# Kernel tuning notes

Measured on AMD Instinct MI355X. Metric: run time of the kernel, lower is better.

The kernel has to match this reference:

```python
import jax, jax.numpy as jnp
import numpy as np

D_MODEL = 1024
HEADS = 16
D_K = D_MODEL // HEADS
D_FF = 4096
EPS = 1e-5


def _layernorm(x, gamma, beta):
    mu = jnp.mean(x, axis=-1, keepdims=True)
    var = jnp.var(x, axis=-1, keepdims=True)
    return (x - mu) * jax.lax.rsqrt(var + EPS) * gamma + beta


def setup_inputs() -> dict:
    key = jax.random.key(0)
    ks = jax.random.split(key, 8)
    s = 0.02
    return {
        "x": jax.random.normal(ks[0], (4, 2048, D_MODEL), dtype=jnp.float32),
        "wq": jax.random.normal(ks[1], (D_MODEL, D_MODEL), dtype=jnp.float32) * s,
        "wk": jax.random.normal(ks[2], (D_MODEL, D_MODEL), dtype=jnp.float32) * s,
        "wv": jax.random.normal(ks[3], (D_MODEL, D_MODEL), dtype=jnp.float32) * s,
        "wo": jax.random.normal(ks[4], (D_MODEL, D_MODEL), dtype=jnp.float32) * s,
        "w1": jax.random.normal(ks[5], (D_MODEL, D_FF), dtype=jnp.float32) * s,
        "b1": jnp.zeros((D_FF,), dtype=jnp.float32),
        "w2": jax.random.normal(ks[6], (D_FF, D_MODEL), dtype=jnp.float32) * s,
        "b2": jnp.zeros((D_MODEL,), dtype=jnp.float32),
        "g1": jnp.ones((D_MODEL,), dtype=jnp.float32),
        "be1": jnp.zeros((D_MODEL,), dtype=jnp.float32),
        "g2": jnp.ones((D_MODEL,), dtype=jnp.float32),
        "be2": jnp.zeros((D_MODEL,), dtype=jnp.float32),
    }


def reference(x, wq, wk, wv, wo, w1, b1, w2, b2, g1, be1, g2, be2):
    B, S, D = x.shape
    # --- multi-head self-attention (dropout = identity at eval) ---
    q = (x @ wq).reshape(B, S, HEADS, D_K).transpose(0, 2, 1, 3)  # [B,H,S,dk]
    k = (x @ wk).reshape(B, S, HEADS, D_K).transpose(0, 2, 1, 3)
    v = (x @ wv).reshape(B, S, HEADS, D_K).transpose(0, 2, 1, 3)
    scores = jnp.einsum("bhqd,bhkd->bhqk", q, k) / jnp.sqrt(jnp.float32(D_K))
    attn = jax.nn.softmax(scores, axis=-1)
    ctx = jnp.einsum("bhqk,bhkd->bhqd", attn, v)
    ctx = ctx.transpose(0, 2, 1, 3).reshape(B, S, D)
    attn_out = ctx @ wo
    # --- add & norm 1 ---
    h = _layernorm(x + attn_out, g1, be1)
    # --- FFN ---
    ffn = jax.nn.relu(h @ w1 + b1) @ w2 + b2
    # --- add & norm 2 ---
    return _layernorm(h + ffn, g2, be2)
```

## Files before the change

kernel.cpp:

```cpp
#include <hip/hip_runtime.h>
#include <hip/hip_bf16.h>


typedef float  floatx2  __attribute__((ext_vector_type(2)));
typedef float  floatx4  __attribute__((ext_vector_type(4)));
typedef float  floatx16 __attribute__((ext_vector_type(16)));
typedef short  shortx8  __attribute__((ext_vector_type(8)));
typedef short  shortx4  __attribute__((ext_vector_type(4)));
typedef int    intx4    __attribute__((ext_vector_type(4)));
typedef unsigned uintx2 __attribute__((ext_vector_type(2)));

__device__ __forceinline__ short f2bs(float f) {
    union { float f; unsigned u; } a; a.f = f;
    unsigned r = a.u + 0x7fffu + ((a.u >> 16) & 1u);
    return (short)(r >> 16);
}

__device__ __forceinline__ float fexp2(float x) {
#if __has_builtin(__builtin_amdgcn_exp2f)
    return __builtin_amdgcn_exp2f(x);
#else
    return __expf(0.6931471805599453f * x);
#endif
}

__device__ __forceinline__ void lane32swap(unsigned& a, unsigned& b) {
#if __has_builtin(__builtin_amdgcn_permlane32_swap)
    uintx2 r = __builtin_amdgcn_permlane32_swap(a, b, false, false);
    a = r[0]; b = r[1];
#else
    int hl = (threadIdx.x & 63) >> 5;
    unsigned ta = (unsigned)__shfl_xor((int)a, 32);
    unsigned tb = (unsigned)__shfl_xor((int)b, 32);
    unsigned na = hl ? tb : a;
    unsigned nb = hl ? b : ta;
    a = na; b = nb;
#endif
}

__device__ __forceinline__ void gload16(const short* g, short* l) {
    __builtin_amdgcn_global_load_lds(
        (const __attribute__((address_space(1))) void*)g,
        (__attribute__((address_space(3))) void*)l,
        16, 0, 0);
}

#define WAITV(n) asm volatile("s_waitcnt vmcnt(" #n ")" ::: "memory")
#define FENCE    asm volatile("" ::: "memory")

__device__ __forceinline__ void trans_tile(const float* __restrict__ in,
                                           short* __restrict__ out,
                                           int N, int K, int k0, int n0,
                                           short (*t)[68]) {
    const int tid = threadIdx.x;
    const int r = tid >> 4, c4 = (tid & 15) * 4;
#pragma unroll
    for (int i = 0; i < 4; ++i) {
        int k = r + i * 16;
        floatx4 v = *(const floatx4*)(in + (size_t)(k0 + k) * N + n0 + c4);
        shortx4 s;
#pragma unroll
        for (int j = 0; j < 4; ++j) s[j] = f2bs(v[j]);
        *(shortx4*)(&t[k][c4]) = s;
    }
    __syncthreads();
#pragma unroll
    for (int i = 0; i < 4; ++i) {
        int n = r + i * 16;
        shortx4 s;
#pragma unroll
        for (int j = 0; j < 4; ++j) s[j] = t[c4 + j][n];
        *(shortx4*)(out + (size_t)(n0 + n) * K + k0 + c4) = s;
    }
}

__global__ __launch_bounds__(256) void prep_kernel(
    const float* __restrict__ wq, const float* __restrict__ wk,
    const float* __restrict__ wv, const float* __restrict__ wo,
    const float* __restrict__ w1, const float* __restrict__ w2,
    const float* __restrict__ x,
    short* wqt, short* wkt, short* wvt, short* wot,
    short* w1t, short* w2t, short* xb)
{
    __shared__ __align__(16) short t[64][68];
    const int bid = blockIdx.x;
    if (bid < 1024) {
        const int widx = bid >> 8, local = bid & 255;
        const float* in = widx == 0 ? wq : widx == 1 ? wk : widx == 2 ? wv : wo;
        short* out = widx == 0 ? wqt : widx == 1 ? wkt : widx == 2 ? wvt : wot;
        trans_tile(in, out, 1024, 1024, (local & 15) * 64, (local >> 4) * 64, t);
    } else if (bid < 2048) {
        const int local = bid - 1024;
        trans_tile(w1, w1t, 4096, 1024, (local & 15) * 64, (local >> 4) * 64, t);
    } else if (bid < 3072) {
        const int local = bid - 2048;
        trans_tile(w2, w2t, 1024, 4096, (local & 63) * 64, (local >> 6) * 64, t);
    } else {
        const int local = bid - 3072;
#pragma unroll
        for (int j = 0; j < 4; ++j) {
            int i = local * 1024 + j * 256 + threadIdx.x;
            floatx4 v = *(const floatx4*)(x + (size_t)i * 4);
            shortx4 o;
            o[0] = f2bs(v[0]); o[1] = f2bs(v[1]); o[2] = f2bs(v[2]); o[3] = f2bs(v[3]);
            *(shortx4*)(xb + (size_t)i * 4) = o;
        }
    }
}

template<int EPI>
__global__ __launch_bounds__(256) void gemm_bt(
    const short* __restrict__ A, const short* __restrict__ Bt, int K, int N,
    short* __restrict__ outb, float* __restrict__ outf,
    const float* __restrict__ bias, const float* __restrict__ resf)
{
    __shared__ __align__(16) short As[2 * 128 * 32];
    __shared__ __align__(16) short Bs[2 * 128 * 32];
    const int tid = threadIdx.x;
    const int bx = blockIdx.x, by = blockIdx.y;
    const int w = tid >> 6, lane = tid & 63, quad = lane >> 4, l16 = lane & 15;
    const int wm = (w >> 1) * 64, wn = (w & 1) * 64;
    const int lr = lane >> 2, lc = (lane & 3) * 8;
    const short* aSrc = A + (size_t)(by * 128 + w * 32 + lr) * K + lc;
    const short* bSrc = Bt + (size_t)(bx * 128 + w * 32 + lr) * K + lc;
    const size_t k16 = (size_t)16 * K;
    const int wb = w * 32 * 32;

    floatx4 acc[4][4] = {};

    gload16(aSrc, As + wb);
    gload16(aSrc + k16, As + wb + 512);
    gload16(bSrc, Bs + wb);
    gload16(bSrc + k16, Bs + wb + 512);

    int cur = 0;
    for (int k0 = 0; k0 < K; k0 += 32) {
        __syncthreads();
        const int kn = k0 + 32;
        if (kn < K) {
            const int nb = (cur ^ 1) * 4096;
            gload16(aSrc + kn, As + nb + wb);
            gload16(aSrc + k16 + kn, As + nb + wb + 512);
            gload16(bSrc + kn, Bs + nb + wb);
            gload16(bSrc + k16 + kn, Bs + nb + wb + 512);
        }
        const short* Ab = As + cur * 4096;
        const short* Bb = Bs + cur * 4096;
        shortx8 af[4], bf[4];
#pragma unroll
        for (int mt = 0; mt < 4; ++mt)
            af[mt] = *(const shortx8*)(Ab + (wm + mt * 16 + l16) * 32 + quad * 8);
#pragma unroll
        for (int nt = 0; nt < 4; ++nt)
            bf[nt] = *(const shortx8*)(Bb + (wn + nt * 16 + l16) * 32 + quad * 8);
#pragma unroll
        for (int mt = 0; mt < 4; ++mt)
#pragma unroll
            for (int nt = 0; nt < 4; ++nt)
                acc[mt][nt] = __builtin_amdgcn_mfma_f32_16x16x32_bf16(af[mt], bf[nt], acc[mt][nt], 0, 0, 0);
        cur ^= 1;
    }

#pragma unroll
    for (int mt = 0; mt < 4; ++mt) {
#pragma unroll
        for (int nt = 0; nt < 4; ++nt) {
            const int grow0 = by * 128 + wm + mt * 16 + quad * 4;
            const int gcol = bx * 128 + wn + nt * 16 + l16;
#pragma unroll
            for (int r = 0; r < 4; ++r) {
                int grow = grow0 + r;
                float v = acc[mt][nt][r];
                if constexpr (EPI == 1) {
                    v += bias[gcol];
                    v = fmaxf(v, 0.f);
                    outb[(size_t)grow * N + gcol] = f2bs(v);
                } else if constexpr (EPI == 2) {
                    outf[(size_t)grow * N + gcol] = v + resf[(size_t)grow * N + gcol];
                } else if constexpr (EPI == 3) {
                    outf[(size_t)grow * N + gcol] = v + bias[gcol] + resf[(size_t)grow * N + gcol];
                }
            }
        }
    }
}

template<int EPI>
__global__ __launch_bounds__(512, 2) void gemm256(
    const short* __restrict__ A, const short* __restrict__ Bt, const int K, const int N,
    short* __restrict__ outb, float* __restrict__ outf,
    const float* __restrict__ bias, const float* __restrict__ resf)
{
    __shared__ __align__(16) short Ls[65536];
    const int tid = threadIdx.x;
    const int w = tid >> 6, lane = tid & 63;
    const int quad = lane >> 4, l16 = lane & 15;
    const int wm = w >> 2, wn = w & 3;
    const int bx = blockIdx.x, by = blockIdx.y;

    const int srow = w * 16 + (lane >> 3);
    const int uc0 = ((lane & 7) ^ ((lane >> 4) & 7)) * 8;
    const int uc1 = ((lane & 7) ^ (((lane >> 4) + 4) & 7)) * 8;
    const short* aS0 = A  + (size_t)(by * 256 + srow) * K + uc0;
    const short* aS1 = A  + (size_t)(by * 256 + srow + 8) * K + uc1;
    const short* bS0 = Bt + (size_t)(bx * 256 + srow) * K + uc0;
    const short* bS1 = Bt + (size_t)(bx * 256 + srow + 8) * K + uc1;
    const size_t hK = (size_t)128 * K;
    const int wsl = w * 1024;

    const int rswz = (l16 >> 1) & 7;
    const int ru0 = (quad ^ rswz) * 8;
    const int ru1 = ((4 + quad) ^ rswz) * 8;
    const int aRd = (wm * 64 + l16) * 64;
    const int bRd = (wn * 32 + l16) * 64;

    floatx4 acc[8][4] = {};
    shortx8 af[4][2], blo[2][2], bhi[2][2];

#define S_A0(buf, kc) { short* p = Ls + (buf) * 32768 + wsl;         gload16(aS0 + (kc), p);      gload16(aS1 + (kc), p + 512);      FENCE; }
#define S_A1(buf, kc) { short* p = Ls + (buf) * 32768 + 8192 + wsl;  gload16(aS0 + hK + (kc), p); gload16(aS1 + hK + (kc), p + 512); FENCE; }
#define S_B0(buf, kc) { short* p = Ls + (buf) * 32768 + 16384 + wsl; gload16(bS0 + (kc), p);      gload16(bS1 + (kc), p + 512);      FENCE; }
#define S_B1(buf, kc) { short* p = Ls + (buf) * 32768 + 24576 + wsl; gload16(bS0 + hK + (kc), p); gload16(bS1 + hK + (kc), p + 512); FENCE; }
#define MF(a, b, c) c = __builtin_amdgcn_mfma_f32_16x16x32_bf16(a, b, c, 0, 0, 0)

    S_A0(0, 0) S_B0(0, 0) S_B1(0, 0) S_A1(0, 0)

    const int NT = K >> 6;
    for (int t = 0; t < NT - 1; ++t) {
        const int rb = t & 1, wbuf = rb ^ 1, kc = (t + 1) * 64;
        const short* Ab = Ls + rb * 32768;
        const short* Bb = Ab + 16384;
        WAITV(4); __builtin_amdgcn_s_barrier(); FENCE;
#pragma unroll
        for (int mf = 0; mf < 4; ++mf) {
            af[mf][0] = *(const shortx8*)(Ab + aRd + mf * 1024 + ru0);
            af[mf][1] = *(const shortx8*)(Ab + aRd + mf * 1024 + ru1);
        }
#pragma unroll
        for (int nf = 0; nf < 2; ++nf) {
            blo[nf][0] = *(const shortx8*)(Bb + bRd + nf * 1024 + ru0);
            blo[nf][1] = *(const shortx8*)(Bb + bRd + nf * 1024 + ru1);
        }
        S_A0(wbuf, kc)
        __builtin_amdgcn_s_setprio(1);
#pragma unroll
        for (int mf = 0; mf < 4; ++mf)
#pragma unroll
            for (int nf = 0; nf < 2; ++nf) {
                MF(af[mf][0], blo[nf][0], acc[mf][nf]);
                MF(af[mf][1], blo[nf][1], acc[mf][nf]);
            }
        __builtin_amdgcn_s_setprio(0);
        WAITV(4); __builtin_amdgcn_s_barrier(); FENCE;
#pragma unroll
        for (int nf = 0; nf < 2; ++nf) {
            bhi[nf][0] = *(const shortx8*)(Bb + bRd + 8192 + nf * 1024 + ru0);
            bhi[nf][1] = *(const shortx8*)(Bb + bRd + 8192 + nf * 1024 + ru1);
        }
        S_B0(wbuf, kc)
        __builtin_amdgcn_s_setprio(1);
#pragma unroll
        for (int mf = 0; mf < 4; ++mf)
#pragma unroll
            for (int nf = 0; nf < 2; ++nf) {
                MF(af[mf][0], bhi[nf][0], acc[mf][2 + nf]);
                MF(af[mf][1], bhi[nf][1], acc[mf][2 + nf]);
            }
        __builtin_amdgcn_s_setprio(0);
        WAITV(4); __builtin_amdgcn_s_barrier(); FENCE;
#pragma unroll
        for (int mf = 0; mf < 4; ++mf) {
            af[mf][0] = *(const shortx8*)(Ab + aRd + 8192 + mf * 1024 + ru0);
            af[mf][1] = *(const shortx8*)(Ab + aRd + 8192 + mf * 1024 + ru1);
        }
        S_B1(wbuf, kc)
        __builtin_amdgcn_s_setprio(1);
#pragma unroll
        for (int mf = 0; mf < 4; ++mf)
#pragma unroll
            for (int nf = 0; nf < 2; ++nf) {
                MF(af[mf][0], blo[nf][0], acc[4 + mf][nf]);
                MF(af[mf][1], blo[nf][1], acc[4 + mf][nf]);
            }
        __builtin_amdgcn_s_setprio(0);
        S_A1(wbuf, kc)
        __builtin_amdgcn_s_setprio(1);
#pragma unroll
        for (int mf = 0; mf < 4; ++mf)
#pragma unroll
            for (int nf = 0; nf < 2; ++nf) {
                MF(af[mf][0], bhi[nf][0], acc[4 + mf][2 + nf]);
                MF(af[mf][1], bhi[nf][1], acc[4 + mf][2 + nf]);
            }
        __builtin_amdgcn_s_setprio(0);
    }
    {
        const int rb = (NT - 1) & 1;
        const short* Ab = Ls + rb * 32768;
        const short* Bb = Ab + 16384;
        WAITV(4); __builtin_amdgcn_s_barrier(); FENCE;
#pragma unroll
        for (int mf = 0; mf < 4; ++mf) {
            af[mf][0] = *(const shortx8*)(Ab + aRd + mf * 1024 + ru0);
            af[mf][1] = *(const shortx8*)(Ab + aRd + mf * 1024 + ru1);
        }
#pragma unroll
        for (int nf = 0; nf < 2; ++nf) {
            blo[nf][0] = *(const shortx8*)(Bb + bRd + nf * 1024 + ru0);
            blo[nf][1] = *(const shortx8*)(Bb + bRd + nf * 1024 + ru1);
        }
        __builtin_amdgcn_s_setprio(1);
#pragma unroll
        for (int mf = 0; mf < 4; ++mf)
#pragma unroll
            for (int nf = 0; nf < 2; ++nf) {
                MF(af[mf][0], blo[nf][0], acc[mf][nf]);
                MF(af[mf][1], blo[nf][1], acc[mf][nf]);
            }
        __builtin_amdgcn_s_setprio(0);
        WAITV(2); __builtin_amdgcn_s_barrier(); FENCE;
#pragma unroll
        for (int nf = 0; nf < 2; ++nf) {
            bhi[nf][0] = *(const shortx8*)(Bb + bRd + 8192 + nf * 1024 + ru0);
            bhi[nf][1] = *(const shortx8*)(Bb + bRd + 8192 + nf * 1024 + ru1);
        }
        __builtin_amdgcn_s_setprio(1);
#pragma unroll
        for (int mf = 0; mf < 4; ++mf)
#pragma unroll
            for (int nf = 0; nf < 2; ++nf) {
                MF(af[mf][0], bhi[nf][0], acc[mf][2 + nf]);
                MF(af[mf][1], bhi[nf][1], acc[mf][2 + nf]);
            }
        __builtin_amdgcn_s_setprio(0);
        WAITV(0); __builtin_amdgcn_s_barrier(); FENCE;
#pragma unroll
        for (int mf = 0; mf < 4; ++mf) {
            af[mf][0] = *(const shortx8*)(Ab + aRd + 8192 + mf * 1024 + ru0);
            af[mf][1] = *(const shortx8*)(Ab + aRd + 8192 + mf * 1024 + ru1);
        }
        __builtin_amdgcn_s_setprio(1);
#pragma unroll
        for (int mf = 0; mf < 4; ++mf)
#pragma unroll
            for (int nf = 0; nf < 2; ++nf) {
                MF(af[mf][0], blo[nf][0], acc[4 + mf][nf]);
                MF(af[mf][1], blo[nf][1], acc[4 + mf][nf]);
                MF(af[mf][0], bhi[nf][0], acc[4 + mf][2 + nf]);
                MF(af[mf][1], bhi[nf][1], acc[4 + mf][2 + nf]);
            }
        __builtin_amdgcn_s_setprio(0);
    }

#pragma unroll
    for (int mf = 0; mf < 8; ++mf) {
        const int grow0 = by * 256 + (mf >> 2) * 128 + wm * 64 + (mf & 3) * 16 + quad * 4;
#pragma unroll
        for (int nf = 0; nf < 4; ++nf) {
            const int gcol = bx * 256 + (nf >> 1) * 128 + wn * 32 + (nf & 1) * 16 + l16;
            const floatx4 a = acc[mf][nf];
            if constexpr (EPI == 5) {
                const int slice = gcol >> 10, c = gcol & 1023;
                const int hh = c >> 6, d = c & 63;
                const int b = grow0 >> 11, s0 = grow0 & 2047;
                if (slice == 2) {
                    short* vt = outb + ((size_t)16 << 20);
                    shortx4 pkv;
#pragma unroll
                    for (int r = 0; r < 4; ++r) pkv[r] = f2bs(a[r]);
                    *(shortx4*)(vt + ((size_t)((b * 16 + hh) * 64 + d)) * 2048 + s0) = pkv;
                } else {
                    short* dst = slice ? (outb + ((size_t)8 << 20)) : outb;
                    float sc = slice ? 1.f : 0.125f * 1.4426950408889634f;
#pragma unroll
                    for (int r = 0; r < 4; ++r)
                        dst[(((size_t)(b * 16 + hh)) * 2048 + (s0 + r)) * 64 + d] =
                            f2bs(a[r] * sc);
                }
            } else if constexpr (EPI == 1) {
                const float bv = bias[gcol];
#pragma unroll
                for (int r = 0; r < 4; ++r) {
                    float v = fmaxf(a[r] + bv, 0.f);
                    outb[(size_t)(grow0 + r) * N + gcol] = f2bs(v);
                }
            } else if constexpr (EPI == 3) {
                const float bv = bias[gcol];
#pragma unroll
                for (int r = 0; r < 4; ++r)
                    outf[(size_t)(grow0 + r) * N + gcol] =
                        a[r] + bv + resf[(size_t)(grow0 + r) * N + gcol];
            }
        }
    }
#undef S_A0
#undef S_A1
#undef S_B0
#undef S_B1
#undef MF
}

__global__ __launch_bounds__(256) void ln_kernel(
    const float* __restrict__ in, float* __restrict__ outf, short* __restrict__ outb,
    const float* __restrict__ g, const float* __restrict__ be, int writeB)
{
    __shared__ float red[8];
    const int row = blockIdx.x, tid = threadIdx.x;
    const float* p = in + (size_t)row * 1024;
    floatx4 v = *(const floatx4*)(p + tid * 4);
    float s = v[0] + v[1] + v[2] + v[3];
    float q = v[0] * v[0] + v[1] * v[1] + v[2] * v[2] + v[3] * v[3];
#pragma unroll
    for (int off = 32; off; off >>= 1) {
        s += __shfl_xor(s, off);
        q += __shfl_xor(q, off);
    }
    int w = tid >> 6, lane = tid & 63;
    if (lane == 0) { red[w] = s; red[4 + w] = q; }
    __syncthreads();
    s = red[0] + red[1] + red[2] + red[3];
    q = red[4] + red[5] + red[6] + red[7];
    float mean = s * (1.f / 1024.f);
    float var = q * (1.f / 1024.f) - mean * mean;
    float rs = rsqrtf(var + 1e-5f);
    floatx4 gv = *(const floatx4*)(g + tid * 4);
    floatx4 bv = *(const floatx4*)(be + tid * 4);
    floatx4 o4;
#pragma unroll
    for (int i = 0; i < 4; ++i) o4[i] = (v[i] - mean) * rs * gv[i] + bv[i];
    *(floatx4*)(outf + (size_t)row * 1024 + tid * 4) = o4;
    if (writeB) {
        shortx4 ob;
#pragma unroll
        for (int i = 0; i < 4; ++i) ob[i] = f2bs(o4[i]);
        *(shortx4*)(outb + (size_t)row * 1024 + tid * 4) = ob;
    }
}

__global__ __launch_bounds__(256) void attn_kernel(
    const short* __restrict__ Q, const short* __restrict__ K,
    const short* __restrict__ Vt, short* __restrict__ ctx)
{
    __shared__ __align__(16) short Ks[128 * 72];
    __shared__ __align__(16) short Vs[64 * 136];
    const int tid = threadIdx.x;
    const int q0 = blockIdx.x * 128, bh = blockIdx.y;
    const int w = tid >> 6, lane = tid & 63, l31 = lane & 31, hl = lane >> 5;
    const size_t sb = (size_t)bh * 2048 * 64;

    shortx8 qf[4];
#pragma unroll
    for (int ks = 0; ks < 4; ++ks)
        qf[ks] = *(const shortx8*)(Q + sb + (size_t)(q0 + w * 32 + l31) * 64 + ks * 16 + hl * 8);

    const int krow = tid >> 3, kcol = (tid & 7) * 8;
    const int vrow = tid >> 4, vcol = (tid & 15) * 8;

    floatx16 o[2] = {};
    floatx2 rs2 = {0.f, 0.f};

    intx4 kv[4], vv[4];
#pragma unroll
    for (int i = 0; i < 4; ++i) {
        kv[i] = *(const intx4*)(K + sb + (size_t)(i * 32 + krow) * 64 + kcol);
        vv[i] = *(const intx4*)(Vt + sb + (size_t)(i * 16 + vrow) * 2048 + vcol);
    }

    for (int kt = 0; kt < 16; ++kt) {
        __syncthreads();
#pragma unroll
        for (int i = 0; i < 4; ++i) {
            *(intx4*)(Ks + (i * 32 + krow) * 72 + kcol) = kv[i];
            *(intx4*)(Vs + (i * 16 + vrow) * 136 + vcol) = vv[i];
        }
        __syncthreads();
        if (kt < 15) {
            const int kv0 = (kt + 1) * 128;
#pragma unroll
            for (int i = 0; i < 4; ++i) {
                kv[i] = *(const intx4*)(K + sb + (size_t)(kv0 + i * 32 + krow) * 64 + kcol);
                vv[i] = *(const intx4*)(Vt + sb + (size_t)(i * 16 + vrow) * 2048 + kv0 + vcol);
            }
        }

#pragma unroll
        for (int mt = 0; mt < 4; ++mt) {
            floatx16 s = {};
#pragma unroll
            for (int ks = 0; ks < 4; ++ks) {
                shortx8 ak = *(const shortx8*)(Ks + (mt * 32 + l31) * 72 + ks * 16 + hl * 8);
                s = __builtin_amdgcn_mfma_f32_32x32x16_bf16(ak, qf[ks], s, 0, 0, 0);
            }
            floatx2 ps2[8];
#pragma unroll
            for (int i = 0; i < 8; ++i) {
                ps2[i][0] = fexp2(s[2 * i]);
                ps2[i][1] = fexp2(s[2 * i + 1]);
                rs2 += ps2[i];
            }
            unsigned pk[8];
#pragma unroll
            for (int i = 0; i < 8; ++i) {
                union { __hip_bfloat162 h; unsigned u; } cv;
                cv.h = __float22bfloat162_rn(make_float2(ps2[i][0], ps2[i][1]));
                pk[i] = cv.u;
            }
            lane32swap(pk[0], pk[2]);
            lane32swap(pk[1], pk[3]);
            lane32swap(pk[4], pk[6]);
            lane32swap(pk[5], pk[7]);
#pragma unroll
            for (int ksl = 0; ksl < 2; ++ksl) {
                union { unsigned i[4]; shortx8 s8; } fr;
                fr.i[0] = pk[4 * ksl];     fr.i[1] = pk[4 * ksl + 1];
                fr.i[2] = pk[4 * ksl + 2]; fr.i[3] = pk[4 * ksl + 3];
#pragma unroll
                for (int mtd = 0; mtd < 2; ++mtd) {
                    shortx8 av = *(const shortx8*)(Vs + (mtd * 32 + l31) * 136 + mt * 32 + ksl * 16 + hl * 8);
                    o[mtd] = __builtin_amdgcn_mfma_f32_32x32x16_bf16(av, fr.s8, o[mtd], 0, 0, 0);
                }
            }
        }
    }

    float rsum = rs2[0] + rs2[1];
    float tot = rsum + __shfl_xor(rsum, 32);
    float inv = 1.f / tot;

    __syncthreads();
    short* O_lds = Ks;
#pragma unroll
    for (int mtd = 0; mtd < 2; ++mtd)
#pragma unroll
        for (int g = 0; g < 4; ++g) {
            shortx4 p4;
#pragma unroll
            for (int r = 0; r < 4; ++r) p4[r] = f2bs(o[mtd][4 * g + r] * inv);
            *(shortx4*)(O_lds + (w * 32 + l31) * 72 + mtd * 32 + g * 8 + hl * 4) = p4;
        }
    __syncthreads();
    const int b = bh >> 4, head = bh & 15;
#pragma unroll
    for (int it = 0; it < 4; ++it) {
        int idx = it * 256 + tid;
        int q = idx >> 3, ch = idx & 7;
        shortx8 v = *(const shortx8*)(O_lds + q * 72 + ch * 8);
        *(shortx8*)(ctx + ((size_t)(b * 2048 + q0 + q)) * 1024 + head * 64 + ch * 8) = v;
    }
}

extern "C" void kernel_launch(void* const* d_in, const int* in_sizes, int n_in,
                              void* d_out, int out_size, void* d_ws, size_t ws_size,
                              hipStream_t stream) {
    const float* x   = (const float*)d_in[0];
    const float* wq  = (const float*)d_in[1];
    const float* wk  = (const float*)d_in[2];
    const float* wv  = (const float*)d_in[3];
    const float* wo  = (const float*)d_in[4];
    const float* w1  = (const float*)d_in[5];
    const float* b1  = (const float*)d_in[6];
    const float* w2  = (const float*)d_in[7];
    const float* b2  = (const float*)d_in[8];
    const float* g1p = (const float*)d_in[9];
    const float* be1 = (const float*)d_in[10];
    const float* g2p = (const float*)d_in[11];
    const float* be2 = (const float*)d_in[12];
    float* out = (float*)d_out;

    char* ws = (char*)d_ws;
    const size_t MB = 1ull << 20;
    short* wqt  = (short*)(ws + 0 * MB);
    short* wkt  = (short*)(ws + 2 * MB);
    short* wvt  = (short*)(ws + 4 * MB);
    short* wot  = (short*)(ws + 6 * MB);
    short* w1t  = (short*)(ws + 8 * MB);
    short* w2t  = (short*)(ws + 16 * MB);
    short* xb   = (short*)(ws + 24 * MB);
    short* Qb   = (short*)(ws + 40 * MB);
    short* Kb   = (short*)(ws + 56 * MB);
    short* Vtg  = (short*)(ws + 72 * MB);
    short* ctxb = (short*)(ws + 88 * MB);
    float* tf   = (float*)(ws + 104 * MB);
    short* hb   = (short*)(ws + 136 * MB);
    short* f1b  = (short*)(ws + 40 * MB);

    prep_kernel<<<5120, 256, 0, stream>>>(wq, wk, wv, wo, w1, w2, x,
                                          wqt, wkt, wvt, wot, w1t, w2t, xb);

    gemm256<5><<<dim3(12, 32), 512, 0, stream>>>(xb, wqt, 1024, 3072, Qb, nullptr, nullptr, nullptr);
    attn_kernel<<<dim3(16, 64), 256, 0, stream>>>(Qb, Kb, Vtg, ctxb);
    gemm_bt<2><<<dim3(8, 64), 256, 0, stream>>>(ctxb, wot, 1024, 1024, nullptr, tf, nullptr, x);
    ln_kernel<<<8192, 256, 0, stream>>>(tf, tf, hb, g1p, be1, 1);
    gemm256<1><<<dim3(16, 32), 512, 0, stream>>>(hb, w1t, 1024, 4096, f1b, nullptr, b1, nullptr);
    gemm256<3><<<dim3(4, 32), 512, 0, stream>>>(f1b, w2t, 4096, 1024, nullptr, out, b2, tf);
    ln_kernel<<<8192, 256, 0, stream>>>(out, out, nullptr, g2p, be2, 0);
}
```

Baseline: 413.7 us.

## Add 256x128 GEMM tile variant, drop gemm_bt, software-pipeline attention QK MFMAs

Templates the 256-wide GEMM on tile width N and adds a 256x128 variant with its own load schedule. The QKV, output-projection and FFN2 GEMMs switch to it so the grid has more blocks across the CUs, and the output projection moves off the older 128x128 kernel. Separately, the attention kernel computes the next QK score tile while the softmax and PV MFMAs of the current tile run, with setprio hints and split row-sum accumulators. This adds overlap and occupancy but raises register pressure and lowers per-block reuse of A tiles.

```diff
diff --git a/kernel.cpp b/kernel.cpp
--- a/kernel.cpp
+++ b/kernel.cpp
@@ -108,90 +108,15 @@
     }
 }
 
-template<int EPI>
-__global__ __launch_bounds__(256) void gemm_bt(
-    const short* __restrict__ A, const short* __restrict__ Bt, int K, int N,
-    short* __restrict__ outb, float* __restrict__ outf,
-    const float* __restrict__ bias, const float* __restrict__ resf)
-{
-    __shared__ __align__(16) short As[2 * 128 * 32];
-    __shared__ __align__(16) short Bs[2 * 128 * 32];
-    const int tid = threadIdx.x;
-    const int bx = blockIdx.x, by = blockIdx.y;
-    const int w = tid >> 6, lane = tid & 63, quad = lane >> 4, l16 = lane & 15;
-    const int wm = (w >> 1) * 64, wn = (w & 1) * 64;
-    const int lr = lane >> 2, lc = (lane & 3) * 8;
-    const short* aSrc = A + (size_t)(by * 128 + w * 32 + lr) * K + lc;
-    const short* bSrc = Bt + (size_t)(bx * 128 + w * 32 + lr) * K + lc;
-    const size_t k16 = (size_t)16 * K;
-    const int wb = w * 32 * 32;
-
-    floatx4 acc[4][4] = {};
-
-    gload16(aSrc, As + wb);
-    gload16(aSrc + k16, As + wb + 512);
-    gload16(bSrc, Bs + wb);
-    gload16(bSrc + k16, Bs + wb + 512);
-
-    int cur = 0;
-    for (int k0 = 0; k0 < K; k0 += 32) {
-        __syncthreads();
-        const int kn = k0 + 32;
-        if (kn < K) {
-            const int nb = (cur ^ 1) * 4096;
-            gload16(aSrc + kn, As + nb + wb);
-            gload16(aSrc + k16 + kn, As + nb + wb + 512);
-            gload16(bSrc + kn, Bs + nb + wb);
-            gload16(bSrc + k16 + kn, Bs + nb + wb + 512);
-        }
-        const short* Ab = As + cur * 4096;
-        const short* Bb = Bs + cur * 4096;
-        shortx8 af[4], bf[4];
-#pragma unroll
-        for (int mt = 0; mt < 4; ++mt)
-            af[mt] = *(const shortx8*)(Ab + (wm + mt * 16 + l16) * 32 + quad * 8);
-#pragma unroll
-        for (int nt = 0; nt < 4; ++nt)
-            bf[nt] = *(const shortx8*)(Bb + (wn + nt * 16 + l16) * 32 + quad * 8);
-#pragma unroll
-        for (int mt = 0; mt < 4; ++mt)
-#pragma unroll
-            for (int nt = 0; nt < 4; ++nt)
-                acc[mt][nt] = __builtin_amdgcn_mfma_f32_16x16x32_bf16(af[mt], bf[nt], acc[mt][nt], 0, 0, 0);
-        cur ^= 1;
-    }
-
-#pragma unroll
-    for (int mt = 0; mt < 4; ++mt) {
-#pragma unroll
-        for (int nt = 0; nt < 4; ++nt) {
-            const int grow0 = by * 128 + wm + mt * 16 + quad * 4;
-            const int gcol = bx * 128 + wn + nt * 16 + l16;
-#pragma unroll
-            for (int r = 0; r < 4; ++r) {
-                int grow = grow0 + r;
-                float v = acc[mt][nt][r];
-                if constexpr (EPI == 1) {
-                    v += bias[gcol];
-                    v = fmaxf(v, 0.f);
-                    outb[(size_t)grow * N + gcol] = f2bs(v);
-                } else if constexpr (EPI == 2) {
-                    outf[(size_t)grow * N + gcol] = v + resf[(size_t)grow * N + gcol];
-                } else if constexpr (EPI == 3) {
-                    outf[(size_t)grow * N + gcol] = v + bias[gcol] + resf[(size_t)grow * N + gcol];
-                }
-            }
-        }
-    }
-}
-
-template<int EPI>
+template<int EPI, int BN>
 __global__ __launch_bounds__(512, 2) void gemm256(
     const short* __restrict__ A, const short* __restrict__ Bt, const int K, const int N,
     short* __restrict__ outb, float* __restrict__ outf,
     const float* __restrict__ bias, const float* __restrict__ resf)
 {
-    __shared__ __align__(16) short Ls[65536];
+    constexpr int BUFSZ = 16384 + BN * 64;
+    constexpr int NF = BN / 64;
+    __shared__ __align__(16) short Ls[2 * BUFSZ];
     const int tid = threadIdx.x;
     const int w = tid >> 6, lane = tid & 63;
     const int quad = lane >> 4, l16 = lane & 15;
@@ -203,8 +128,8 @@
     const int uc1 = ((lane & 7) ^ (((lane >> 4) + 4) & 7)) * 8;
     const short* aS0 = A  + (size_t)(by * 256 + srow) * K + uc0;
     const short* aS1 = A  + (size_t)(by * 256 + srow + 8) * K + uc1;
-    const short* bS0 = Bt + (size_t)(bx * 256 + srow) * K + uc0;
-    const short* bS1 = Bt + (size_t)(bx * 256 + srow + 8) * K + uc1;
+    const short* bS0 = Bt + (size_t)(bx * BN + srow) * K + uc0;
+    const short* bS1 = Bt + (size_t)(bx * BN + srow + 8) * K + uc1;
     const size_t hK = (size_t)128 * K;
     const int wsl = w * 1024;
 
@@ -214,150 +139,240 @@
     const int aRd = (wm * 64 + l16) * 64;
     const int bRd = (wn * 32 + l16) * 64;
 
-    floatx4 acc[8][4] = {};
+    floatx4 acc[8][NF] = {};
     shortx8 af[4][2], blo[2][2], bhi[2][2];
 
-#define S_A0(buf, kc) { short* p = Ls + (buf) * 32768 + wsl;         gload16(aS0 + (kc), p);      gload16(aS1 + (kc), p + 512);      FENCE; }
-#define S_A1(buf, kc) { short* p = Ls + (buf) * 32768 + 8192 + wsl;  gload16(aS0 + hK + (kc), p); gload16(aS1 + hK + (kc), p + 512); FENCE; }
-#define S_B0(buf, kc) { short* p = Ls + (buf) * 32768 + 16384 + wsl; gload16(bS0 + (kc), p);      gload16(bS1 + (kc), p + 512);      FENCE; }
-#define S_B1(buf, kc) { short* p = Ls + (buf) * 32768 + 24576 + wsl; gload16(bS0 + hK + (kc), p); gload16(bS1 + hK + (kc), p + 512); FENCE; }
+#define S_A0(buf, kc) { short* p = Ls + (buf) * BUFSZ + wsl;         gload16(aS0 + (kc), p);      gload16(aS1 + (kc), p + 512);      FENCE; }
+#define S_A1(buf, kc) { short* p = Ls + (buf) * BUFSZ + 8192 + wsl;  gload16(aS0 + hK + (kc), p); gload16(aS1 + hK + (kc), p + 512); FENCE; }
+#define S_B0(buf, kc) { short* p = Ls + (buf) * BUFSZ + 16384 + wsl; gload16(bS0 + (kc), p);      gload16(bS1 + (kc), p + 512);      FENCE; }
+#define S_B1(buf, kc) { short* p = Ls + (buf) * BUFSZ + 24576 + wsl; gload16(bS0 + hK + (kc), p); gload16(bS1 + hK + (kc), p + 512); FENCE; }
 #define MF(a, b, c) c = __builtin_amdgcn_mfma_f32_16x16x32_bf16(a, b, c, 0, 0, 0)
 
-    S_A0(0, 0) S_B0(0, 0) S_B1(0, 0) S_A1(0, 0)
-
     const int NT = K >> 6;
-    for (int t = 0; t < NT - 1; ++t) {
-        const int rb = t & 1, wbuf = rb ^ 1, kc = (t + 1) * 64;
-        const short* Ab = Ls + rb * 32768;
-        const short* Bb = Ab + 16384;
-        WAITV(4); __builtin_amdgcn_s_barrier(); FENCE;
-#pragma unroll
-        for (int mf = 0; mf < 4; ++mf) {
-            af[mf][0] = *(const shortx8*)(Ab + aRd + mf * 1024 + ru0);
-            af[mf][1] = *(const shortx8*)(Ab + aRd + mf * 1024 + ru1);
-        }
-#pragma unroll
-        for (int nf = 0; nf < 2; ++nf) {
-            blo[nf][0] = *(const shortx8*)(Bb + bRd + nf * 1024 + ru0);
-            blo[nf][1] = *(const shortx8*)(Bb + bRd + nf * 1024 + ru1);
-        }
-        S_A0(wbuf, kc)
-        __builtin_amdgcn_s_setprio(1);
-#pragma unroll
-        for (int mf = 0; mf < 4; ++mf)
+
+    if constexpr (BN == 256) {
+        S_A0(0, 0) S_B0(0, 0) S_B1(0, 0) S_A1(0, 0)
+        for (int t = 0; t < NT - 1; ++t) {
+            const int rb = t & 1, wbuf = rb ^ 1, kc = (t + 1) * 64;
+            const short* Ab = Ls + rb * BUFSZ;
+            const short* Bb = Ab + 16384;
+            WAITV(4); __builtin_amdgcn_s_barrier(); FENCE;
+#pragma unroll
+            for (int mf = 0; mf < 4; ++mf) {
+                af[mf][0] = *(const shortx8*)(Ab + aRd + mf * 1024 + ru0);
+                af[mf][1] = *(const shortx8*)(Ab + aRd + mf * 1024 + ru1);
+            }
 #pragma unroll
             for (int nf = 0; nf < 2; ++nf) {
-                MF(af[mf][0], blo[nf][0], acc[mf][nf]);
-                MF(af[mf][1], blo[nf][1], acc[mf][nf]);
-            }
-        __builtin_amdgcn_s_setprio(0);
-        WAITV(4); __builtin_amdgcn_s_barrier(); FENCE;
-#pragma unroll
-        for (int nf = 0; nf < 2; ++nf) {
-            bhi[nf][0] = *(const shortx8*)(Bb + bRd + 8192 + nf * 1024 + ru0);
-            bhi[nf][1] = *(const shortx8*)(Bb + bRd + 8192 + nf * 1024 + ru1);
-        }
-        S_B0(wbuf, kc)
-        __builtin_amdgcn_s_setprio(1);
-#pragma unroll
-        for (int mf = 0; mf < 4; ++mf)
+                blo[nf][0] = *(const shortx8*)(Bb + bRd + nf * 1024 + ru0);
+                blo[nf][1] = *(const shortx8*)(Bb + bRd + nf * 1024 + ru1);
+            }
+            S_A0(wbuf, kc)
+            __builtin_amdgcn_s_setprio(1);
+#pragma unroll
+            for (int mf = 0; mf < 4; ++mf)
+#pragma unroll
+                for (int nf = 0; nf < 2; ++nf) {
+                    MF(af[mf][0], blo[nf][0], acc[mf][nf]);
+                    MF(af[mf][1], blo[nf][1], acc[mf][nf]);
+                }
+            __builtin_amdgcn_s_setprio(0);
+            WAITV(4); __builtin_amdgcn_s_barrier(); FENCE;
 #pragma unroll
             for (int nf = 0; nf < 2; ++nf) {
-                MF(af[mf][0], bhi[nf][0], acc[mf][2 + nf]);
-                MF(af[mf][1], bhi[nf][1], acc[mf][2 + nf]);
-            }
-        __builtin_amdgcn_s_setprio(0);
-        WAITV(4); __builtin_amdgcn_s_barrier(); FENCE;
-#pragma unroll
-        for (int mf = 0; mf < 4; ++mf) {
-            af[mf][0] = *(const shortx8*)(Ab + aRd + 8192 + mf * 1024 + ru0);
-            af[mf][1] = *(const shortx8*)(Ab + aRd + 8192 + mf * 1024 + ru1);
-        }
-        S_B1(wbuf, kc)
-        __builtin_amdgcn_s_setprio(1);
-#pragma unroll
-        for (int mf = 0; mf < 4; ++mf)
+                bhi[nf][0] = *(const shortx8*)(Bb + bRd + 8192 + nf * 1024 + ru0);
+                bhi[nf][1] = *(const shortx8*)(Bb + bRd + 8192 + nf * 1024 + ru1);
+            }
+            S_B0(wbuf, kc)
+            __builtin_amdgcn_s_setprio(1);
+#pragma unroll
+            for (int mf = 0; mf < 4; ++mf)
+#pragma unroll
+                for (int nf = 0; nf < 2; ++nf) {
+                    MF(af[mf][0], bhi[nf][0], acc[mf][2 + nf]);
+                    MF(af[mf][1], bhi[nf][1], acc[mf][2 + nf]);
+                }
+            __builtin_amdgcn_s_setprio(0);
+            WAITV(4); __builtin_amdgcn_s_barrier(); FENCE;
+#pragma unroll
+            for (int mf = 0; mf < 4; ++mf) {
+                af[mf][0] = *(const shortx8*)(Ab + aRd + 8192 + mf * 1024 + ru0);
+                af[mf][1] = *(const shortx8*)(Ab + aRd + 8192 + mf * 1024 + ru1);
+            }
+            S_B1(wbuf, kc)
+            __builtin_amdgcn_s_setprio(1);
+#pragma unroll
+            for (int mf = 0; mf < 4; ++mf)
+#pragma unroll
+                for (int nf = 0; nf < 2; ++nf) {
+                    MF(af[mf][0], blo[nf][0], acc[4 + mf][nf]);
+                    MF(af[mf][1], blo[nf][1], acc[4 + mf][nf]);
+                }
+            __builtin_amdgcn_s_setprio(0);
+            S_A1(wbuf, kc)
+            __builtin_amdgcn_s_setprio(1);
+#pragma unroll
+            for (int mf = 0; mf < 4; ++mf)
+#pragma unroll
+                for (int nf = 0; nf < 2; ++nf) {
+                    MF(af[mf][0], bhi[nf][0], acc[4 + mf][2 + nf]);
+                    MF(af[mf][1], bhi[nf][1], acc[4 + mf][2 + nf]);
+                }
+            __builtin_amdgcn_s_setprio(0);
+        }
+        {
+            const int rb = (NT - 1) & 1;
+            const short* Ab = Ls + rb * BUFSZ;
+            const short* Bb = Ab + 16384;
+            WAITV(4); __builtin_amdgcn_s_barrier(); FENCE;
+#pragma unroll
+            for (int mf = 0; mf < 4; ++mf) {
+                af[mf][0] = *(const shortx8*)(Ab + aRd + mf * 1024 + ru0);
+                af[mf][1] = *(const shortx8*)(Ab + aRd + mf * 1024 + ru1);
+            }
 #pragma unroll
             for (int nf = 0; nf < 2; ++nf) {
-                MF(af[mf][0], blo[nf][0], acc[4 + mf][nf]);
-                MF(af[mf][1], blo[nf][1], acc[4 + mf][nf]);
-            }
-        __builtin_amdgcn_s_setprio(0);
-        S_A1(wbuf, kc)
-        __builtin_amdgcn_s_setprio(1);
-#pragma unroll
-        for (int mf = 0; mf < 4; ++mf)
+                blo[nf][0] = *(const shortx8*)(Bb + bRd + nf * 1024 + ru0);
+                blo[nf][1] = *(const shortx8*)(Bb + bRd + nf * 1024 + ru1);
+            }
+            __builtin_amdgcn_s_setprio(1);
+#pragma unroll
+            for (int mf = 0; mf < 4; ++mf)
+#pragma unroll
+                for (int nf = 0; nf < 2; ++nf) {
+                    MF(af[mf][0], blo[nf][0], acc[mf][nf]);
+                    MF(af[mf][1], blo[nf][1], acc[mf][nf]);
+                }
+            __builtin_amdgcn_s_setprio(0);
+            WAITV(2); __builtin_amdgcn_s_barrier(); FENCE;
 #pragma unroll
             for (int nf = 0; nf < 2; ++nf) {
-                MF(af[mf][0], bhi[nf][0], acc[4 + mf][2 + nf]);
-                MF(af[mf][1], bhi[nf][1], acc[4 + mf][2 + nf]);
-            }
-        __builtin_amdgcn_s_setprio(0);
-    }
-    {
-        const int rb = (NT - 1) & 1;
-        const short* Ab = Ls + rb * 32768;
-        const short* Bb = Ab + 16384;
-        WAITV(4); __builtin_amdgcn_s_barrier(); FENCE;
-#pragma unroll
-        for (int mf = 0; mf < 4; ++mf) {
-            af[mf][0] = *(const shortx8*)(Ab + aRd + mf * 1024 + ru0);
-            af[mf][1] = *(const shortx8*)(Ab + aRd + mf * 1024 + ru1);
-        }
-#pragma unroll
-        for (int nf = 0; nf < 2; ++nf) {
-            blo[nf][0] = *(const shortx8*)(Bb + bRd + nf * 1024 + ru0);
-            blo[nf][1] = *(const shortx8*)(Bb + bRd + nf * 1024 + ru1);
-        }
-        __builtin_amdgcn_s_setprio(1);
-#pragma unroll
-        for (int mf = 0; mf < 4; ++mf)
+                bhi[nf][0] = *(const shortx8*)(Bb + bRd + 8192 + nf * 1024 + ru0);
+                bhi[nf][1] = *(const shortx8*)(Bb + bRd + 8192 + nf * 1024 + ru1);
+            }
+            __builtin_amdgcn_s_setprio(1);
+#pragma unroll
+            for (int mf = 0; mf < 4; ++mf)
+#pragma unroll
+                for (int nf = 0; nf < 2; ++nf) {
+                    MF(af[mf][0], bhi[nf][0], acc[mf][2 + nf]);
+                    MF(af[mf][1], bhi[nf][1], acc[mf][2 + nf]);
+                }
+            __builtin_amdgcn_s_setprio(0);
+            WAITV(0); __builtin_amdgcn_s_barrier(); FENCE;
+#pragma unroll
+            for (int mf = 0; mf < 4; ++mf) {
+                af[mf][0] = *(const shortx8*)(Ab + aRd + 8192 + mf * 1024 + ru0);
+                af[mf][1] = *(const shortx8*)(Ab + aRd + 8192 + mf * 1024 + ru1);
+            }
+            __builtin_amdgcn_s_setprio(1);
+#pragma unroll
+            for (int mf = 0; mf < 4; ++mf)
+#pragma unroll
+                for (int nf = 0; nf < 2; ++nf) {
+                    MF(af[mf][0], blo[nf][0], acc[4 + mf][nf]);
+                    MF(af[mf][1], blo[nf][1], acc[4 + mf][nf]);
+                    MF(af[mf][0], bhi[nf][0], acc[4 + mf][2 + nf]);
+                    MF(af[mf][1], bhi[nf][1], acc[4 + mf][2 + nf]);
+                }
+            __builtin_amdgcn_s_setprio(0);
+        }
+    } else {
+        S_A0(0, 0) S_B0(0, 0) S_A1(0, 0)
+        for (int t = 0; t < NT - 1; ++t) {
+            const int rb = t & 1, wbuf = rb ^ 1, kc = (t + 1) * 64;
+            const short* Ab = Ls + rb * BUFSZ;
+            const short* Bb = Ab + 16384;
+            WAITV(2); __builtin_amdgcn_s_barrier(); FENCE;
+#pragma unroll
+            for (int mf = 0; mf < 4; ++mf) {
+                af[mf][0] = *(const shortx8*)(Ab + aRd + mf * 1024 + ru0);
+                af[mf][1] = *(const shortx8*)(Ab + aRd + mf * 1024 + ru1);
+            }
 #pragma unroll
             for (int nf = 0; nf < 2; ++nf) {
-                MF(af[mf][0], blo[nf][0], acc[mf][nf]);
-                MF(af[mf][1], blo[nf][1], acc[mf][nf]);
-            }
-        __builtin_amdgcn_s_setprio(0);
-        WAITV(2); __builtin_amdgcn_s_barrier(); FENCE;
-#pragma unroll
-        for (int nf = 0; nf < 2; ++nf) {
-            bhi[nf][0] = *(const shortx8*)(Bb + bRd + 8192 + nf * 1024 + ru0);
-            bhi[nf][1] = *(const shortx8*)(Bb + bRd + 8192 + nf * 1024 + ru1);
-        }
-        __builtin_amdgcn_s_setprio(1);
-#pragma unroll
-        for (int mf = 0; mf < 4; ++mf)
+                blo[nf][0] = *(const shortx8*)(Bb + bRd + nf * 1024 + ru0);
+                blo[nf][1] = *(const shortx8*)(Bb + bRd + nf * 1024 + ru1);
+            }
+            S_A0(wbuf, kc)
+            __builtin_amdgcn_s_setprio(1);
+#pragma unroll
+            for (int mf = 0; mf < 4; ++mf)
+#pragma unroll
+                for (int nf = 0; nf < 2; ++nf) {
+                    MF(af[mf][0], blo[nf][0], acc[mf][nf]);
+                    MF(af[mf][1], blo[nf][1], acc[mf][nf]);
+                }
+            __builtin_amdgcn_s_setprio(0);
+            WAITV(2); __builtin_amdgcn_s_barrier(); FENCE;
+#pragma unroll
+            for (int mf = 0; mf < 4; ++mf) {
+                af[mf][0] = *(const shortx8*)(Ab + aRd + 8192 + mf * 1024 + ru0);
+                af[mf][1] = *(const shortx8*)(Ab + aRd + 8192 + mf * 1024 + ru1);
+            }
+            S_B0(wbuf, kc) S_A1(wbuf, kc)
+            __builtin_amdgcn_s_setprio(1);
+#pragma unroll
+            for (int mf = 0; mf < 4; ++mf)
+#pragma unroll
+                for (int nf = 0; nf < 2; ++nf) {
+                    MF(af[mf][0], blo[nf][0], acc[4 + mf][nf]);
+                    MF(af[mf][1], blo[nf][1], acc[4 + mf][nf]);
+                }
+            __builtin_amdgcn_s_setprio(0);
+        }
+        {
+            const int rb = (NT - 1) & 1;
+            const short* Ab = Ls + rb * BUFSZ;
+            const short* Bb = Ab + 16384;
+            WAITV(2); __builtin_amdgcn_s_barrier(); FENCE;
+#pragma unroll
+            for (int mf = 0; mf < 4; ++mf) {
+                af[mf][0] = *(const shortx8*)(Ab + aRd + mf * 1024 + ru0);
+                af[mf][1] = *(const shortx8*)(Ab + aRd + mf * 1024 + ru1);
+            }
 #pragma unroll
             for (int nf = 0; nf < 2; ++nf) {
-                MF(af[mf][0], bhi[nf][0], acc[mf][2 + nf]);
-                MF(af[mf][1], bhi[nf][1], acc[mf][2 + nf]);
-            }
-        __builtin_amdgcn_s_setprio(0);
-        WAITV(0); __builtin_amdgcn_s_barrier(); FENCE;
-#pragma unroll
-        for (int mf = 0; mf < 4; ++mf) {
-            af[mf][0] = *(const shortx8*)(Ab + aRd + 8192 + mf * 1024 + ru0);
-            af[mf][1] = *(const shortx8*)(Ab + aRd + 8192 + mf * 1024 + ru1);
-        }
-        __builtin_amdgcn_s_setprio(1);
-#pragma unroll
-        for (int mf = 0; mf < 4; ++mf)
-#pragma unroll
-            for (int nf = 0; nf < 2; ++nf) {
-                MF(af[mf][0], blo[nf][0], acc[4 + mf][nf]);
-                MF(af[mf][1], blo[nf][1], acc[4 + mf][nf]);
-                MF(af[mf][0], bhi[nf][0], acc[4 + mf][2 + nf]);
-                MF(af[mf][1], bhi[nf][1], acc[4 + mf][2 + nf]);
-            }
-        __builtin_amdgcn_s_setprio(0);
+                blo[nf][0] = *(const shortx8*)(Bb + bRd + nf * 1024 + ru0);
+                blo[nf][1] = *(const shortx8*)(Bb + bRd + nf * 1024 + ru1);
+            }
+            __builtin_amdgcn_s_setprio(1);
+#pragma unroll
+            for (int mf = 0; mf < 4; ++mf)
+#pragma unroll
+                for (int nf = 0; nf < 2; ++nf) {
+                    MF(af[mf][0], blo[nf][0], acc[mf][nf]);
+                    MF(af[mf][1], blo[nf][1], acc[mf][nf]);
+                }
+            __builtin_amdgcn_s_setprio(0);
+            WAITV(0); __builtin_amdgcn_s_barrier(); FENCE;
+#pragma unroll
+            for (int mf = 0; mf < 4; ++mf) {
+                af[mf][0] = *(const shortx8*)(Ab + aRd + 8192 + mf * 1024 + ru0);
+                af[mf][1] = *(const shortx8*)(Ab + aRd + 8192 + mf * 1024 + ru1);
+            }
+            __builtin_amdgcn_s_setprio(1);
+#pragma unroll
+            for (int mf = 0; mf < 4; ++mf)
+#pragma unroll
+                for (int nf = 0; nf < 2; ++nf) {
+                    MF(af[mf][0], blo[nf][0], acc[4 + mf][nf]);
+                    MF(af[mf][1], blo[nf][1], acc[4 + mf][nf]);
+                }
+            __builtin_amdgcn_s_setprio(0);
+        }
     }
 
 #pragma unroll
     for (int mf = 0; mf < 8; ++mf) {
         const int grow0 = by * 256 + (mf >> 2) * 128 + wm * 64 + (mf & 3) * 16 + quad * 4;
 #pragma unroll
-        for (int nf = 0; nf < 4; ++nf) {
-            const int gcol = bx * 256 + (nf >> 1) * 128 + wn * 32 + (nf & 1) * 16 + l16;
+        for (int nf = 0; nf < NF; ++nf) {
+            int gcol;
+            if constexpr (BN == 256)
+                gcol = bx * 256 + (nf >> 1) * 128 + wn * 32 + (nf & 1) * 16 + l16;
+            else
+                gcol = bx * 128 + wn * 32 + nf * 16 + l16;
             const floatx4 a = acc[mf][nf];
             if constexpr (EPI == 5) {
                 const int slice = gcol >> 10, c = gcol & 1023;
@@ -384,6 +399,11 @@
                     float v = fmaxf(a[r] + bv, 0.f);
                     outb[(size_t)(grow0 + r) * N + gcol] = f2bs(v);
                 }
+            } else if constexpr (EPI == 2) {
+#pragma unroll
+                for (int r = 0; r < 4; ++r)
+                    outf[(size_t)(grow0 + r) * N + gcol] =
+                        a[r] + resf[(size_t)(grow0 + r) * N + gcol];
             } else if constexpr (EPI == 3) {
                 const float bv = bias[gcol];
 #pragma unroll
@@ -457,7 +477,8 @@
     const int vrow = tid >> 4, vcol = (tid & 15) * 8;
 
     floatx16 o[2] = {};
-    floatx2 rs2 = {0.f, 0.f};
+    floatx2 rsA = {0.f, 0.f}, rsB = {0.f, 0.f};
+    const floatx16 z = {};
 
     intx4 kv[4], vv[4];
 #pragma unroll
@@ -466,6 +487,9 @@
         vv[i] = *(const intx4*)(Vt + sb + (size_t)(i * 16 + vrow) * 2048 + vcol);
     }
 
+#define LD_AK(mt, ks) (*(const shortx8*)(Ks + ((mt) * 32 + l31) * 72 + (ks) * 16 + hl * 8))
+#define LD_AV(mtd, mt, ksl) (*(const shortx8*)(Vs + ((mtd) * 32 + l31) * 136 + (mt) * 32 + (ksl) * 16 + hl * 8))
+
     for (int kt = 0; kt < 16; ++kt) {
         __syncthreads();
 #pragma unroll
@@ -483,21 +507,34 @@
             }
         }
 
+        floatx16 sc;
+        {
+            __builtin_amdgcn_s_setprio(1);
+            sc = __builtin_amdgcn_mfma_f32_32x32x16_bf16(LD_AK(0, 0), qf[0], z, 0, 0, 0);
+            sc = __builtin_amdgcn_mfma_f32_32x32x16_bf16(LD_AK(0, 1), qf[1], sc, 0, 0, 0);
+            sc = __builtin_amdgcn_mfma_f32_32x32x16_bf16(LD_AK(0, 2), qf[2], sc, 0, 0, 0);
+            sc = __builtin_amdgcn_mfma_f32_32x32x16_bf16(LD_AK(0, 3), qf[3], sc, 0, 0, 0);
+            __builtin_amdgcn_s_setprio(0);
+        }
 #pragma unroll
         for (int mt = 0; mt < 4; ++mt) {
-            floatx16 s = {};
-#pragma unroll
-            for (int ks = 0; ks < 4; ++ks) {
-                shortx8 ak = *(const shortx8*)(Ks + (mt * 32 + l31) * 72 + ks * 16 + hl * 8);
-                s = __builtin_amdgcn_mfma_f32_32x32x16_bf16(ak, qf[ks], s, 0, 0, 0);
+            floatx16 sn;
+            if (mt < 3) {
+                __builtin_amdgcn_s_setprio(1);
+                sn = __builtin_amdgcn_mfma_f32_32x32x16_bf16(LD_AK(mt + 1, 0), qf[0], z, 0, 0, 0);
+                sn = __builtin_amdgcn_mfma_f32_32x32x16_bf16(LD_AK(mt + 1, 1), qf[1], sn, 0, 0, 0);
+                sn = __builtin_amdgcn_mfma_f32_32x32x16_bf16(LD_AK(mt + 1, 2), qf[2], sn, 0, 0, 0);
+                sn = __builtin_amdgcn_mfma_f32_32x32x16_bf16(LD_AK(mt + 1, 3), qf[3], sn, 0, 0, 0);
+                __builtin_amdgcn_s_setprio(0);
             }
             floatx2 ps2[8];
 #pragma unroll
             for (int i = 0; i < 8; ++i) {
-                ps2[i][0] = fexp2(s[2 * i]);
-                ps2[i][1] = fexp2(s[2 * i + 1]);
-                rs2 += ps2[i];
-            }
+                ps2[i][0] = fexp2(sc[2 * i]);
+                ps2[i][1] = fexp2(sc[2 * i + 1]);
+            }
+#pragma unroll
+            for (int i = 0; i < 8; i += 2) { rsA += ps2[i]; rsB += ps2[i + 1]; }
             unsigned pk[8];
 #pragma unroll
             for (int i = 0; i < 8; ++i) {
@@ -509,21 +546,24 @@
             lane32swap(pk[1], pk[3]);
             lane32swap(pk[4], pk[6]);
             lane32swap(pk[5], pk[7]);
+            __builtin_amdgcn_s_setprio(1);
 #pragma unroll
             for (int ksl = 0; ksl < 2; ++ksl) {
                 union { unsigned i[4]; shortx8 s8; } fr;
                 fr.i[0] = pk[4 * ksl];     fr.i[1] = pk[4 * ksl + 1];
                 fr.i[2] = pk[4 * ksl + 2]; fr.i[3] = pk[4 * ksl + 3];
 #pragma unroll
-                for (int mtd = 0; mtd < 2; ++mtd) {
-                    shortx8 av = *(const shortx8*)(Vs + (mtd * 32 + l31) * 136 + mt * 32 + ksl * 16 + hl * 8);
-                    o[mtd] = __builtin_amdgcn_mfma_f32_32x32x16_bf16(av, fr.s8, o[mtd], 0, 0, 0);
-                }
-            }
-        }
-    }
-
-    float rsum = rs2[0] + rs2[1];
+                for (int mtd = 0; mtd < 2; ++mtd)
+                    o[mtd] = __builtin_amdgcn_mfma_f32_32x32x16_bf16(LD_AV(mtd, mt, ksl), fr.s8, o[mtd], 0, 0, 0);
+            }
+            __builtin_amdgcn_s_setprio(0);
+            if (mt < 3) sc = sn;
+        }
+    }
+#undef LD_AK
+#undef LD_AV
+
+    float rsum = rsA[0] + rsA[1] + rsB[0] + rsB[1];
     float tot = rsum + __shfl_xor(rsum, 32);
     float inv = 1.f / tot;
 
@@ -587,11 +627,11 @@
     prep_kernel<<<5120, 256, 0, stream>>>(wq, wk, wv, wo, w1, w2, x,
                                           wqt, wkt, wvt, wot, w1t, w2t, xb);
 
-    gemm256<5><<<dim3(12, 32), 512, 0, stream>>>(xb, wqt, 1024, 3072, Qb, nullptr, nullptr, nullptr);
+    gemm256<5, 128><<<dim3(24, 32), 512, 0, stream>>>(xb, wqt, 1024, 3072, Qb, nullptr, nullptr, nullptr);
     attn_kernel<<<dim3(16, 64), 256, 0, stream>>>(Qb, Kb, Vtg, ctxb);
-    gemm_bt<2><<<dim3(8, 64), 256, 0, stream>>>(ctxb, wot, 1024, 1024, nullptr, tf, nullptr, x);
+    gemm256<2, 128><<<dim3(8, 32), 512, 0, stream>>>(ctxb, wot, 1024, 1024, nullptr, tf, nullptr, x);
     ln_kernel<<<8192, 256, 0, stream>>>(tf, tf, hb, g1p, be1, 1);
-    gemm256<1><<<dim3(16, 32), 512, 0, stream>>>(hb, w1t, 1024, 4096, f1b, nullptr, b1, nullptr);
-    gemm256<3><<<dim3(4, 32), 512, 0, stream>>>(f1b, w2t, 4096, 1024, nullptr, out, b2, tf);
+    gemm256<1, 256><<<dim3(16, 32), 512, 0, stream>>>(hb, w1t, 1024, 4096, f1b, nullptr, b1, nullptr);
+    gemm256<3, 128><<<dim3(8, 32), 512, 0, stream>>>(f1b, w2t, 4096, 1024, nullptr, out, b2, tf);
     ln_kernel<<<8192, 256, 0, stream>>>(out, out, nullptr, g2p, be2, 0);
 }
```

Result: no change. 410.5 us (-0.8%).
